# Optimization experiments

Measured on AMD Instinct MI355X. Metric: run time of the kernel, lower is better.

Reference implementation:

```python
import jax, jax.numpy as jnp
import numpy as np

EMBED_DIM = 128
N_CLASSES = 5
NX = 1024
NY = 1024


def setup_inputs() -> dict:
    key = jax.random.key(0)
    k1, k2 = jax.random.split(key)
    z_x = jax.random.normal(k1, (NX, EMBED_DIM), dtype=jnp.float32)
    z_y = jax.random.normal(k2, (NY, EMBED_DIM), dtype=jnp.float32)
    # Parameter init exactly as in __init__ for the L1 compare
    ex = 2 * np.sqrt(2 / np.pi) * EMBED_DIM
    var = 4 * (1 - 2 / np.pi) * EMBED_DIM
    beta_init = ex / np.sqrt(var)
    theta = jnp.ones((1, N_CLASSES - 1), dtype=jnp.float32) / np.sqrt(var)  # clamped >=0, already positive
    beta = jnp.full((N_CLASSES - 1,), beta_init, dtype=jnp.float32)
    return {"z_x": z_x, "z_y": z_y, "theta": theta, "beta": beta}


def reference(z_x, z_y, theta, beta):
    # L1 compare: s[i,j] = -sum_d |z_x[i,d] - z_y[j,d]|   -> (Nx, Ny)
    s = -jnp.sum(jnp.abs(z_x[:, None, :] - z_y[None, :, :]), axis=-1)
    # SSA: dual softmax soft alignment
    a = jax.nn.softmax(s, axis=1)  # row softmax
    b = jax.nn.softmax(s, axis=0)  # column softmax
    a = a + b - a * b
    a = a / jnp.sum(a)
    # weighted reduction -> scalar similarity
    c = jnp.sum(a * s)
    logits = c * theta + beta  # (1, n_classes-1) broadcast
    return logits.reshape(-1)
```

## Files before the change

### kernel.cpp

```cpp
#include <hip/hip_runtime.h>
#include <math.h>

#define NXC 1024
#define NYC 1024
#define DC  128
#define NCM1 4
#define NBLK 256

#define WS_STILE 0
#define WS_ROWP  1048576
#define WS_COLP  1081344
#define WS_PART  1114112

typedef _Float16 half2v __attribute__((ext_vector_type(2)));
union H2U { half2v h; unsigned u; };

#if defined(__has_builtin)
#if __has_builtin(__builtin_amdgcn_fdot2)
#define HAVE_FDOT2 1
#endif
#endif

__device__ __forceinline__ float absdiff_dot(uint4 xa, uint4 ya, float acc)
{
    const unsigned* xu = (const unsigned*)&xa;
    const unsigned* yu = (const unsigned*)&ya;
    half2v one; one.x = (_Float16)1.f; one.y = (_Float16)1.f;
    #pragma unroll
    for (int q = 0; q < 4; ++q) {
        H2U x, y, d;
        x.u = xu[q]; y.u = yu[q];
        d.h = x.h - y.h;
        d.u &= 0x7FFF7FFFu;
#ifdef HAVE_FDOT2
        acc = __builtin_amdgcn_fdot2(d.h, one, acc, false);
#else
        acc += (float)d.h.x + (float)d.h.y;
#endif
    }
    return acc;
}

__global__ __launch_bounds__(512, 2) void distance_kernel(
    const float* __restrict__ zx, const float* __restrict__ zy,
    float* __restrict__ ws)
{
    __shared__ __align__(16) _Float16 xs[64 * 128];
    __shared__ __align__(16) _Float16 ys[64 * 128];
    __shared__ float cpm[32][64], cpl[32][64];

    float* stile = ws + WS_STILE;
    float* rowp  = ws + WS_ROWP;
    float* colp  = ws + WS_COLP;

    const int t  = threadIdx.x;
    const int bx = blockIdx.x & 15;
    const int by = blockIdx.x >> 4;
    const int x0 = by * 64;
    const int y0 = bx * 64;

    #pragma unroll
    for (int k = 0; k < 2; ++k) {
        int idx = t + k * 512;
        int r   = idx >> 4;
        int j   = idx & 15;
        int off = r * 128 + 8 * (j ^ ((r >> 2) & 7));

        const float4* gx = (const float4*)(zx + (size_t)(x0 + r) * DC + 8 * j);
        float4 xv0 = gx[0], xv1 = gx[1];
        const float4* gy = (const float4*)(zy + (size_t)(y0 + r) * DC + 8 * j);
        float4 yv0 = gy[0], yv1 = gy[1];

        uint4 hx, hy;
        {
            H2U a, b, c, d;
            a.h.x = (_Float16)xv0.x; a.h.y = (_Float16)xv0.y;
            b.h.x = (_Float16)xv0.z; b.h.y = (_Float16)xv0.w;
            c.h.x = (_Float16)xv1.x; c.h.y = (_Float16)xv1.y;
            d.h.x = (_Float16)xv1.z; d.h.y = (_Float16)xv1.w;
            hx.x = a.u; hx.y = b.u; hx.z = c.u; hx.w = d.u;
            a.h.x = (_Float16)yv0.x; a.h.y = (_Float16)yv0.y;
            b.h.x = (_Float16)yv0.z; b.h.y = (_Float16)yv0.w;
            c.h.x = (_Float16)yv1.x; c.h.y = (_Float16)yv1.y;
            d.h.x = (_Float16)yv1.z; d.h.y = (_Float16)yv1.w;
            hy.x = a.u; hy.y = b.u; hy.z = c.u; hy.w = d.u;
        }
        *(uint4*)(xs + off) = hx;
        *(uint4*)(ys + off) = hy;
    }
    __syncthreads();

    const int tx = t & 15;
    const int ty = t >> 4;
    const int xswz = (ty >> 1) & 7;
    const int yswz = tx & 7;

    const _Float16* xb = xs + (2 * ty) * 128;
    const _Float16* yb = ys + (4 * tx) * 128;

    float acc[2][4];
    #pragma unroll
    for (int i = 0; i < 2; ++i)
        #pragma unroll
        for (int j = 0; j < 4; ++j) acc[i][j] = 0.f;

    uint4 xc0 = *(const uint4*)(xb +       8 * (0 ^ xswz));
    uint4 xc1 = *(const uint4*)(xb + 128 + 8 * (0 ^ xswz));
    uint4 yc0 = *(const uint4*)(yb +       8 * (0 ^ yswz));
    uint4 yc1 = *(const uint4*)(yb + 128 + 8 * (0 ^ yswz));
    uint4 yc2 = *(const uint4*)(yb + 256 + 8 * (0 ^ yswz));
    uint4 yc3 = *(const uint4*)(yb + 384 + 8 * (0 ^ yswz));

    #pragma unroll 4
    for (int j = 0; j < 16; ++j) {
        uint4 xa0 = xc0, xa1 = xc1, ya0 = yc0, ya1 = yc1, ya2 = yc2, ya3 = yc3;
        if (j < 15) {
            const int jn = j + 1;
            xc0 = *(const uint4*)(xb +       8 * (jn ^ xswz));
            xc1 = *(const uint4*)(xb + 128 + 8 * (jn ^ xswz));
            yc0 = *(const uint4*)(yb +       8 * (jn ^ yswz));
            yc1 = *(const uint4*)(yb + 128 + 8 * (jn ^ yswz));
            yc2 = *(const uint4*)(yb + 256 + 8 * (jn ^ yswz));
            yc3 = *(const uint4*)(yb + 384 + 8 * (jn ^ yswz));
        }
        acc[0][0] = absdiff_dot(xa0, ya0, acc[0][0]);
        acc[0][1] = absdiff_dot(xa0, ya1, acc[0][1]);
        acc[0][2] = absdiff_dot(xa0, ya2, acc[0][2]);
        acc[0][3] = absdiff_dot(xa0, ya3, acc[0][3]);
        acc[1][0] = absdiff_dot(xa1, ya0, acc[1][0]);
        acc[1][1] = absdiff_dot(xa1, ya1, acc[1][1]);
        acc[1][2] = absdiff_dot(xa1, ya2, acc[1][2]);
        acc[1][3] = absdiff_dot(xa1, ya3, acc[1][3]);
    }

    float sv[2][4];
    #pragma unroll
    for (int i = 0; i < 2; ++i)
        #pragma unroll
        for (int j = 0; j < 4; ++j) sv[i][j] = -acc[i][j];

    {
        float* sb = stile + (size_t)blockIdx.x * 4096 + t * 8;
        *(float4*)(sb)     = make_float4(sv[0][0], sv[0][1], sv[0][2], sv[0][3]);
        *(float4*)(sb + 4) = make_float4(sv[1][0], sv[1][1], sv[1][2], sv[1][3]);
    }

    #pragma unroll
    for (int i = 0; i < 2; ++i) {
        float m = fmaxf(fmaxf(sv[i][0], sv[i][1]), fmaxf(sv[i][2], sv[i][3]));
        float l = __expf(sv[i][0] - m) + __expf(sv[i][1] - m)
                + __expf(sv[i][2] - m) + __expf(sv[i][3] - m);
        #pragma unroll
        for (int off = 1; off < 16; off <<= 1) {
            float mo = __shfl_xor(m, off, 64);
            float lo = __shfl_xor(l, off, 64);
            float nm = fmaxf(m, mo);
            l = l * __expf(m - nm) + lo * __expf(mo - nm);
            m = nm;
        }
        if (tx == 0)
            *(float2*)(rowp + 2 * ((size_t)(x0 + 2 * ty + i) * 16 + bx)) = make_float2(m, l);
    }

    #pragma unroll
    for (int j = 0; j < 4; ++j) {
        float m = fmaxf(sv[0][j], sv[1][j]);
        float l = __expf(sv[0][j] - m) + __expf(sv[1][j] - m);
        cpm[ty][4 * tx + j] = m;
        cpl[ty][4 * tx + j] = l;
    }
    __syncthreads();
    if (t < 64) {
        float m = cpm[0][t], l = cpl[0][t];
        #pragma unroll 8
        for (int k = 1; k < 32; ++k) {
            float mo = cpm[k][t], lo = cpl[k][t];
            float nm = fmaxf(m, mo);
            l = l * __expf(m - nm) + lo * __expf(mo - nm);
            m = nm;
        }
        *(float2*)(colp + 2 * ((size_t)(y0 + t) * 16 + by)) = make_float2(m, l);
    }
}

__global__ __launch_bounds__(512, 2) void reduce_kernel(
    const float* __restrict__ ws_in, float* __restrict__ ws_out)
{
    __shared__ float rm_s[64], rl_s[64], cm_s[64], cl_s[64];
    __shared__ float red0[8], red1[8];

    const float* stile = ws_in + WS_STILE;
    const float* rowp  = ws_in + WS_ROWP;
    const float* colp  = ws_in + WS_COLP;
    float* part = ws_out + WS_PART;

    const int t  = threadIdx.x;
    const int bx = blockIdx.x & 15;
    const int by = blockIdx.x >> 4;
    const int x0 = by * 64;
    const int y0 = bx * 64;

    if (t < 64) {
        const float2* base = (const float2*)(rowp) + (size_t)(x0 + t) * 16;
        float2 p = base[0];
        float m = p.x, l = p.y;
        #pragma unroll
        for (int k = 1; k < 16; ++k) {
            float2 q = base[k];
            float nm = fmaxf(m, q.x);
            l = l * __expf(m - nm) + q.y * __expf(q.x - nm);
            m = nm;
        }
        rm_s[t] = m; rl_s[t] = 1.f / l;
    } else if (t < 128) {
        const float2* base = (const float2*)(colp) + (size_t)(y0 + (t - 64)) * 16;
        float2 p = base[0];
        float m = p.x, l = p.y;
        #pragma unroll
        for (int k = 1; k < 16; ++k) {
            float2 q = base[k];
            float nm = fmaxf(m, q.x);
            l = l * __expf(m - nm) + q.y * __expf(q.x - nm);
            m = nm;
        }
        cm_s[t - 64] = m; cl_s[t - 64] = 1.f / l;
    }
    __syncthreads();

    const int tx = t & 15;
    const int ty = t >> 4;

    const float* sb = stile + (size_t)blockIdx.x * 4096 + t * 8;
    float4 s0 = ((const float4*)sb)[0];
    float4 s1 = ((const float4*)sb)[1];
    float sv[2][4] = {{s0.x, s0.y, s0.z, s0.w}, {s1.x, s1.y, s1.z, s1.w}};

    float S0 = 0.f, S1 = 0.f;
    #pragma unroll
    for (int i = 0; i < 2; ++i) {
        const float rm = rm_s[2 * ty + i];
        const float rl = rl_s[2 * ty + i];
        #pragma unroll
        for (int j = 0; j < 4; ++j) {
            const float cm = cm_s[4 * tx + j];
            const float cl = cl_s[4 * tx + j];
            float s = sv[i][j];
            float a = __expf(s - rm) * rl;
            float b = __expf(s - cm) * cl;
            float w = a + b - a * b;
            S0 += w;
            S1 += w * s;
        }
    }
    #pragma unroll
    for (int off = 32; off; off >>= 1) {
        S0 += __shfl_xor(S0, off, 64);
        S1 += __shfl_xor(S1, off, 64);
    }
    {
        const int wave = t >> 6, lane = t & 63;
        if (lane == 0) { red0[wave] = S0; red1[wave] = S1; }
    }
    __syncthreads();
    if (t == 0) {
        float t0 = 0.f, t1 = 0.f;
        #pragma unroll
        for (int w = 0; w < 8; ++w) { t0 += red0[w]; t1 += red1[w]; }
        *(float2*)(part + 2 * blockIdx.x) = make_float2(t0, t1);
    }
}

__global__ __launch_bounds__(256) void finalize_kernel(
    const float* __restrict__ ws,
    const float* __restrict__ theta, const float* __restrict__ beta,
    float* __restrict__ out)
{
    __shared__ float red0[4], red1[4];
    const float* part = ws + WS_PART;
    const int t = threadIdx.x;

    float2 p = ((const float2*)part)[t];
    float S0 = p.x, S1 = p.y;
    #pragma unroll
    for (int off = 32; off; off >>= 1) {
        S0 += __shfl_xor(S0, off, 64);
        S1 += __shfl_xor(S1, off, 64);
    }
    const int wave = t >> 6, lane = t & 63;
    if (lane == 0) { red0[wave] = S0; red1[wave] = S1; }
    __syncthreads();
    if (t < NCM1) {
        float t0 = red0[0] + red0[1] + red0[2] + red0[3];
        float t1 = red1[0] + red1[1] + red1[2] + red1[3];
        float c = t1 / t0;
        out[t] = c * theta[t] + beta[t];
    }
}

extern "C" void kernel_launch(void* const* d_in, const int* in_sizes, int n_in,
                              void* d_out, int out_size, void* d_ws, size_t ws_size,
                              hipStream_t stream)
{
    const float* zx    = (const float*)d_in[0];
    const float* zy    = (const float*)d_in[1];
    const float* theta = (const float*)d_in[2];
    const float* beta  = (const float*)d_in[3];
    float* out = (float*)d_out;
    float* ws  = (float*)d_ws;

    distance_kernel<<<NBLK, 512, 0, stream>>>(zx, zy, ws);
    reduce_kernel<<<NBLK, 512, 0, stream>>>(ws, ws);
    finalize_kernel<<<1, 256, 0, stream>>>(ws, theta, beta, out);
}
```

Measured before the change: 77.15 us.

## Fuse finalize into reduce via last-block atomic counter and parallelize partial merges

New measurement: 81.51 us. 5.6% more time.

```diff
diff --git a/kernel.cpp b/kernel.cpp
--- a/kernel.cpp
+++ b/kernel.cpp
@@ -11,9 +11,11 @@
 #define WS_ROWP  1048576
 #define WS_COLP  1081344
 #define WS_PART  1114112
+#define WS_CNT   1114624
 
 typedef _Float16 half2v __attribute__((ext_vector_type(2)));
 union H2U { half2v h; unsigned u; };
+union F2U { float2 f; unsigned long long u; };
 
 #if defined(__has_builtin)
 #if __has_builtin(__builtin_amdgcn_fdot2)
@@ -58,6 +60,9 @@
     const int by = blockIdx.x >> 4;
     const int x0 = by * 64;
     const int y0 = bx * 64;
+
+    if (blockIdx.x == 0 && t == 0)
+        ((int*)ws)[WS_CNT] = 0;
 
     #pragma unroll
     for (int k = 0; k < 2; ++k) {
@@ -114,15 +119,14 @@
     #pragma unroll 4
     for (int j = 0; j < 16; ++j) {
         uint4 xa0 = xc0, xa1 = xc1, ya0 = yc0, ya1 = yc1, ya2 = yc2, ya3 = yc3;
-        if (j < 15) {
-            const int jn = j + 1;
-            xc0 = *(const uint4*)(xb +       8 * (jn ^ xswz));
-            xc1 = *(const uint4*)(xb + 128 + 8 * (jn ^ xswz));
-            yc0 = *(const uint4*)(yb +       8 * (jn ^ yswz));
-            yc1 = *(const uint4*)(yb + 128 + 8 * (jn ^ yswz));
-            yc2 = *(const uint4*)(yb + 256 + 8 * (jn ^ yswz));
-            yc3 = *(const uint4*)(yb + 384 + 8 * (jn ^ yswz));
-        }
+        const int jn = (j + 1) & 15;
+        xc0 = *(const uint4*)(xb +       8 * (jn ^ xswz));
+        xc1 = *(const uint4*)(xb + 128 + 8 * (jn ^ xswz));
+        yc0 = *(const uint4*)(yb +       8 * (jn ^ yswz));
+        yc1 = *(const uint4*)(yb + 128 + 8 * (jn ^ yswz));
+        yc2 = *(const uint4*)(yb + 256 + 8 * (jn ^ yswz));
+        yc3 = *(const uint4*)(yb + 384 + 8 * (jn ^ yswz));
+
         acc[0][0] = absdiff_dot(xa0, ya0, acc[0][0]);
         acc[0][1] = absdiff_dot(xa0, ya1, acc[0][1]);
         acc[0][2] = absdiff_dot(xa0, ya2, acc[0][2]);
@@ -184,15 +188,19 @@
 }
 
 __global__ __launch_bounds__(512, 2) void reduce_kernel(
-    const float* __restrict__ ws_in, float* __restrict__ ws_out)
+    float* __restrict__ ws,
+    const float* __restrict__ theta, const float* __restrict__ beta,
+    float* __restrict__ out)
 {
     __shared__ float rm_s[64], rl_s[64], cm_s[64], cl_s[64];
     __shared__ float red0[8], red1[8];
-
-    const float* stile = ws_in + WS_STILE;
-    const float* rowp  = ws_in + WS_ROWP;
-    const float* colp  = ws_in + WS_COLP;
-    float* part = ws_out + WS_PART;
+    __shared__ int last_s;
+
+    const float* stile = ws + WS_STILE;
+    const float4* rowp4 = (const float4*)(ws + WS_ROWP);
+    const float4* colp4 = (const float4*)(ws + WS_COLP);
+    float* part = ws + WS_PART;
+    int*   cnt  = (int*)ws + WS_CNT;
 
     const int t  = threadIdx.x;
     const int bx = blockIdx.x & 15;
@@ -200,39 +208,44 @@
     const int x0 = by * 64;
     const int y0 = bx * 64;
 
-    if (t < 64) {
-        const float2* base = (const float2*)(rowp) + (size_t)(x0 + t) * 16;
-        float2 p = base[0];
-        float m = p.x, l = p.y;
-        #pragma unroll
-        for (int k = 1; k < 16; ++k) {
-            float2 q = base[k];
-            float nm = fmaxf(m, q.x);
-            l = l * __expf(m - nm) + q.y * __expf(q.x - nm);
-            m = nm;
-        }
-        rm_s[t] = m; rl_s[t] = 1.f / l;
-    } else if (t < 128) {
-        const float2* base = (const float2*)(colp) + (size_t)(y0 + (t - 64)) * 16;
-        float2 p = base[0];
-        float m = p.x, l = p.y;
-        #pragma unroll
-        for (int k = 1; k < 16; ++k) {
-            float2 q = base[k];
-            float nm = fmaxf(m, q.x);
-            l = l * __expf(m - nm) + q.y * __expf(q.x - nm);
-            m = nm;
-        }
-        cm_s[t - 64] = m; cl_s[t - 64] = 1.f / l;
-    }
-    __syncthreads();
-
-    const int tx = t & 15;
-    const int ty = t >> 4;
-
     const float* sb = stile + (size_t)blockIdx.x * 4096 + t * 8;
     float4 s0 = ((const float4*)sb)[0];
     float4 s1 = ((const float4*)sb)[1];
+
+    const int item  = t >> 3;
+    const int chunk = t & 7;
+    {
+        float4 q = rowp4[(size_t)(x0 + item) * 8 + chunk];
+        float m = fmaxf(q.x, q.z);
+        float l = q.y * __expf(q.x - m) + q.w * __expf(q.z - m);
+        #pragma unroll
+        for (int off = 1; off < 8; off <<= 1) {
+            float mo = __shfl_xor(m, off, 64);
+            float lo = __shfl_xor(l, off, 64);
+            float nm = fmaxf(m, mo);
+            l = l * __expf(m - nm) + lo * __expf(mo - nm);
+            m = nm;
+        }
+        if (chunk == 0) { rm_s[item] = m; rl_s[item] = 1.f / l; }
+    }
+    {
+        float4 q = colp4[(size_t)(y0 + item) * 8 + chunk];
+        float m = fmaxf(q.x, q.z);
+        float l = q.y * __expf(q.x - m) + q.w * __expf(q.z - m);
+        #pragma unroll
+        for (int off = 1; off < 8; off <<= 1) {
+            float mo = __shfl_xor(m, off, 64);
+            float lo = __shfl_xor(l, off, 64);
+            float nm = fmaxf(m, mo);
+            l = l * __expf(m - nm) + lo * __expf(mo - nm);
+            m = nm;
+        }
+        if (chunk == 0) { cm_s[item] = m; cl_s[item] = 1.f / l; }
+    }
+    __syncthreads();
+
+    const int tx = t & 15;
+    const int ty = t >> 4;
     float sv[2][4] = {{s0.x, s0.y, s0.z, s0.w}, {s1.x, s1.y, s1.z, s1.w}};
 
     float S0 = 0.f, S1 = 0.f;
@@ -267,33 +280,36 @@
         #pragma unroll
         for (int w = 0; w < 8; ++w) { t0 += red0[w]; t1 += red1[w]; }
         *(float2*)(part + 2 * blockIdx.x) = make_float2(t0, t1);
-    }
-}
-
-__global__ __launch_bounds__(256) void finalize_kernel(
-    const float* __restrict__ ws,
-    const float* __restrict__ theta, const float* __restrict__ beta,
-    float* __restrict__ out)
-{
-    __shared__ float red0[4], red1[4];
-    const float* part = ws + WS_PART;
-    const int t = threadIdx.x;
-
-    float2 p = ((const float2*)part)[t];
-    float S0 = p.x, S1 = p.y;
-    #pragma unroll
-    for (int off = 32; off; off >>= 1) {
-        S0 += __shfl_xor(S0, off, 64);
-        S1 += __shfl_xor(S1, off, 64);
-    }
-    const int wave = t >> 6, lane = t & 63;
-    if (lane == 0) { red0[wave] = S0; red1[wave] = S1; }
-    __syncthreads();
-    if (t < NCM1) {
-        float t0 = red0[0] + red0[1] + red0[2] + red0[3];
-        float t1 = red1[0] + red1[1] + red1[2] + red1[3];
-        float c = t1 / t0;
-        out[t] = c * theta[t] + beta[t];
+        __threadfence();
+        int old = __hip_atomic_fetch_add(cnt, 1, __ATOMIC_ACQ_REL, __HIP_MEMORY_SCOPE_AGENT);
+        last_s = (old == NBLK - 1);
+    }
+    __syncthreads();
+
+    if (last_s) {
+        float S0f = 0.f, S1f = 0.f;
+        if (t < NBLK) {
+            F2U u;
+            u.u = __hip_atomic_load((const unsigned long long*)(part + 2 * t),
+                                    __ATOMIC_RELAXED, __HIP_MEMORY_SCOPE_AGENT);
+            S0f = u.f.x; S1f = u.f.y;
+        }
+        #pragma unroll
+        for (int off = 32; off; off >>= 1) {
+            S0f += __shfl_xor(S0f, off, 64);
+            S1f += __shfl_xor(S1f, off, 64);
+        }
+        {
+            const int wave = t >> 6, lane = t & 63;
+            if (lane == 0) { red0[wave] = S0f; red1[wave] = S1f; }
+        }
+        __syncthreads();
+        if (t < NCM1) {
+            float t0 = red0[0] + red0[1] + red0[2] + red0[3];
+            float t1 = red1[0] + red1[1] + red1[2] + red1[3];
+            float c = t1 / t0;
+            out[t] = c * theta[t] + beta[t];
+        }
     }
 }
 
@@ -309,6 +325,5 @@
     float* ws  = (float*)d_ws;
 
     distance_kernel<<<NBLK, 512, 0, stream>>>(zx, zy, ws);
-    reduce_kernel<<<NBLK, 512, 0, stream>>>(ws, ws);
-    finalize_kernel<<<1, 256, 0, stream>>>(ws, theta, beta, out);
+    reduce_kernel<<<NBLK, 512, 0, stream>>>(ws, theta, beta, out);
 }
```

## Split distance tiles into half-width blocks and parallelize reduce-stage partial merges

Applied to the files above, without the earlier changes.

Result: no change. 76.67 us (-0.6%).

```diff
diff --git a/kernel.cpp b/kernel.cpp
--- a/kernel.cpp
+++ b/kernel.cpp
@@ -5,12 +5,13 @@
 #define NYC 1024
 #define DC  128
 #define NCM1 4
-#define NBLK 256
+#define NTILE 256
+#define NBLKA 512
 
 #define WS_STILE 0
 #define WS_ROWP  1048576
-#define WS_COLP  1081344
-#define WS_PART  1114112
+#define WS_COLP  1114112
+#define WS_PART  1146880
 
 typedef _Float16 half2v __attribute__((ext_vector_type(2)));
 union H2U { half2v h; unsigned u; };
@@ -41,59 +42,70 @@
     return acc;
 }
 
-__global__ __launch_bounds__(512, 2) void distance_kernel(
+__global__ __launch_bounds__(256, 2) void distance_kernel(
     const float* __restrict__ zx, const float* __restrict__ zy,
     float* __restrict__ ws)
 {
     __shared__ __align__(16) _Float16 xs[64 * 128];
-    __shared__ __align__(16) _Float16 ys[64 * 128];
-    __shared__ float cpm[32][64], cpl[32][64];
+    __shared__ __align__(16) _Float16 ys[32 * 128];
+    __shared__ float cpm[32][32], cpl[32][32];
 
     float* stile = ws + WS_STILE;
     float* rowp  = ws + WS_ROWP;
     float* colp  = ws + WS_COLP;
 
-    const int t  = threadIdx.x;
-    const int bx = blockIdx.x & 15;
-    const int by = blockIdx.x >> 4;
-    const int x0 = by * 64;
-    const int y0 = bx * 64;
-
-    #pragma unroll
-    for (int k = 0; k < 2; ++k) {
-        int idx = t + k * 512;
+    const int t    = threadIdx.x;
+    const int tile = blockIdx.x >> 1;
+    const int h    = blockIdx.x & 1;
+    const int bx   = tile & 15;
+    const int by   = tile >> 4;
+    const int x0   = by * 64;
+    const int y0   = bx * 64 + h * 32;
+
+    #pragma unroll
+    for (int k = 0; k < 4; ++k) {
+        int idx = t + k * 256;
         int r   = idx >> 4;
         int j   = idx & 15;
         int off = r * 128 + 8 * (j ^ ((r >> 2) & 7));
-
         const float4* gx = (const float4*)(zx + (size_t)(x0 + r) * DC + 8 * j);
-        float4 xv0 = gx[0], xv1 = gx[1];
-        const float4* gy = (const float4*)(zy + (size_t)(y0 + r) * DC + 8 * j);
-        float4 yv0 = gy[0], yv1 = gy[1];
-
-        uint4 hx, hy;
+        float4 v0 = gx[0], v1 = gx[1];
+        uint4 hx;
         {
             H2U a, b, c, d;
-            a.h.x = (_Float16)xv0.x; a.h.y = (_Float16)xv0.y;
-            b.h.x = (_Float16)xv0.z; b.h.y = (_Float16)xv0.w;
-            c.h.x = (_Float16)xv1.x; c.h.y = (_Float16)xv1.y;
-            d.h.x = (_Float16)xv1.z; d.h.y = (_Float16)xv1.w;
+            a.h.x = (_Float16)v0.x; a.h.y = (_Float16)v0.y;
+            b.h.x = (_Float16)v0.z; b.h.y = (_Float16)v0.w;
+            c.h.x = (_Float16)v1.x; c.h.y = (_Float16)v1.y;
+            d.h.x = (_Float16)v1.z; d.h.y = (_Float16)v1.w;
             hx.x = a.u; hx.y = b.u; hx.z = c.u; hx.w = d.u;
-            a.h.x = (_Float16)yv0.x; a.h.y = (_Float16)yv0.y;
-            b.h.x = (_Float16)yv0.z; b.h.y = (_Float16)yv0.w;
-            c.h.x = (_Float16)yv1.x; c.h.y = (_Float16)yv1.y;
-            d.h.x = (_Float16)yv1.z; d.h.y = (_Float16)yv1.w;
+        }
+        *(uint4*)(xs + off) = hx;
+    }
+    #pragma unroll
+    for (int k = 0; k < 2; ++k) {
+        int idx = t + k * 256;
+        int r   = idx >> 4;
+        int j   = idx & 15;
+        int off = r * 128 + 8 * (j ^ ((r >> 2) & 7));
+        const float4* gy = (const float4*)(zy + (size_t)(y0 + r) * DC + 8 * j);
+        float4 v0 = gy[0], v1 = gy[1];
+        uint4 hy;
+        {
+            H2U a, b, c, d;
+            a.h.x = (_Float16)v0.x; a.h.y = (_Float16)v0.y;
+            b.h.x = (_Float16)v0.z; b.h.y = (_Float16)v0.w;
+            c.h.x = (_Float16)v1.x; c.h.y = (_Float16)v1.y;
+            d.h.x = (_Float16)v1.z; d.h.y = (_Float16)v1.w;
             hy.x = a.u; hy.y = b.u; hy.z = c.u; hy.w = d.u;
         }
-        *(uint4*)(xs + off) = hx;
         *(uint4*)(ys + off) = hy;
     }
     __syncthreads();
 
-    const int tx = t & 15;
-    const int ty = t >> 4;
+    const int tx = t & 7;
+    const int ty = t >> 3;
     const int xswz = (ty >> 1) & 7;
-    const int yswz = tx & 7;
+    const int yswz = tx;
 
     const _Float16* xb = xs + (2 * ty) * 128;
     const _Float16* yb = ys + (4 * tx) * 128;
@@ -114,15 +126,14 @@
     #pragma unroll 4
     for (int j = 0; j < 16; ++j) {
         uint4 xa0 = xc0, xa1 = xc1, ya0 = yc0, ya1 = yc1, ya2 = yc2, ya3 = yc3;
-        if (j < 15) {
-            const int jn = j + 1;
-            xc0 = *(const uint4*)(xb +       8 * (jn ^ xswz));
-            xc1 = *(const uint4*)(xb + 128 + 8 * (jn ^ xswz));
-            yc0 = *(const uint4*)(yb +       8 * (jn ^ yswz));
-            yc1 = *(const uint4*)(yb + 128 + 8 * (jn ^ yswz));
-            yc2 = *(const uint4*)(yb + 256 + 8 * (jn ^ yswz));
-            yc3 = *(const uint4*)(yb + 384 + 8 * (jn ^ yswz));
-        }
+        const int jn = (j + 1) & 15;
+        xc0 = *(const uint4*)(xb +       8 * (jn ^ xswz));
+        xc1 = *(const uint4*)(xb + 128 + 8 * (jn ^ xswz));
+        yc0 = *(const uint4*)(yb +       8 * (jn ^ yswz));
+        yc1 = *(const uint4*)(yb + 128 + 8 * (jn ^ yswz));
+        yc2 = *(const uint4*)(yb + 256 + 8 * (jn ^ yswz));
+        yc3 = *(const uint4*)(yb + 384 + 8 * (jn ^ yswz));
+
         acc[0][0] = absdiff_dot(xa0, ya0, acc[0][0]);
         acc[0][1] = absdiff_dot(xa0, ya1, acc[0][1]);
         acc[0][2] = absdiff_dot(xa0, ya2, acc[0][2]);
@@ -140,7 +151,7 @@
         for (int j = 0; j < 4; ++j) sv[i][j] = -acc[i][j];
 
     {
-        float* sb = stile + (size_t)blockIdx.x * 4096 + t * 8;
+        float* sb = stile + (size_t)tile * 4096 + h * 2048 + t * 8;
         *(float4*)(sb)     = make_float4(sv[0][0], sv[0][1], sv[0][2], sv[0][3]);
         *(float4*)(sb + 4) = make_float4(sv[1][0], sv[1][1], sv[1][2], sv[1][3]);
     }
@@ -151,7 +162,7 @@
         float l = __expf(sv[i][0] - m) + __expf(sv[i][1] - m)
                 + __expf(sv[i][2] - m) + __expf(sv[i][3] - m);
         #pragma unroll
-        for (int off = 1; off < 16; off <<= 1) {
+        for (int off = 1; off < 8; off <<= 1) {
             float mo = __shfl_xor(m, off, 64);
             float lo = __shfl_xor(l, off, 64);
             float nm = fmaxf(m, mo);
@@ -159,7 +170,7 @@
             m = nm;
         }
         if (tx == 0)
-            *(float2*)(rowp + 2 * ((size_t)(x0 + 2 * ty + i) * 16 + bx)) = make_float2(m, l);
+            *(float2*)(rowp + 2 * ((size_t)(x0 + 2 * ty + i) * 32 + bx * 2 + h)) = make_float2(m, l);
     }
 
     #pragma unroll
@@ -170,7 +181,7 @@
         cpl[ty][4 * tx + j] = l;
     }
     __syncthreads();
-    if (t < 64) {
+    if (t < 32) {
         float m = cpm[0][t], l = cpl[0][t];
         #pragma unroll 8
         for (int k = 1; k < 32; ++k) {
@@ -190,60 +201,76 @@
     __shared__ float red0[8], red1[8];
 
     const float* stile = ws_in + WS_STILE;
-    const float* rowp  = ws_in + WS_ROWP;
-    const float* colp  = ws_in + WS_COLP;
+    const float4* rowp4 = (const float4*)(ws_in + WS_ROWP);
+    const float4* colp4 = (const float4*)(ws_in + WS_COLP);
     float* part = ws_out + WS_PART;
 
-    const int t  = threadIdx.x;
-    const int bx = blockIdx.x & 15;
-    const int by = blockIdx.x >> 4;
-    const int x0 = by * 64;
-    const int y0 = bx * 64;
-
-    if (t < 64) {
-        const float2* base = (const float2*)(rowp) + (size_t)(x0 + t) * 16;
-        float2 p = base[0];
-        float m = p.x, l = p.y;
-        #pragma unroll
-        for (int k = 1; k < 16; ++k) {
-            float2 q = base[k];
-            float nm = fmaxf(m, q.x);
-            l = l * __expf(m - nm) + q.y * __expf(q.x - nm);
-            m = nm;
-        }
-        rm_s[t] = m; rl_s[t] = 1.f / l;
-    } else if (t < 128) {
-        const float2* base = (const float2*)(colp) + (size_t)(y0 + (t - 64)) * 16;
-        float2 p = base[0];
-        float m = p.x, l = p.y;
-        #pragma unroll
-        for (int k = 1; k < 16; ++k) {
-            float2 q = base[k];
-            float nm = fmaxf(m, q.x);
-            l = l * __expf(m - nm) + q.y * __expf(q.x - nm);
-            m = nm;
-        }
-        cm_s[t - 64] = m; cl_s[t - 64] = 1.f / l;
-    }
-    __syncthreads();
-
-    const int tx = t & 15;
-    const int ty = t >> 4;
-
-    const float* sb = stile + (size_t)blockIdx.x * 4096 + t * 8;
+    const int t    = threadIdx.x;
+    const int tile = blockIdx.x;
+    const int bx   = tile & 15;
+    const int by   = tile >> 4;
+    const int x0   = by * 64;
+    const int y0   = bx * 64;
+
+    const float* sb = stile + (size_t)tile * 4096 + t * 8;
     float4 s0 = ((const float4*)sb)[0];
     float4 s1 = ((const float4*)sb)[1];
+
+    const int item  = t >> 3;
+    const int lane8 = t & 7;
+
+    {
+        float4 q0 = rowp4[(size_t)(x0 + item) * 16 + 2 * lane8];
+        float4 q1 = rowp4[(size_t)(x0 + item) * 16 + 2 * lane8 + 1];
+        float m = fmaxf(q0.x, q0.z);
+        float l = q0.y * __expf(q0.x - m) + q0.w * __expf(q0.z - m);
+        float m2 = fmaxf(q1.x, q1.z);
+        float l2 = q1.y * __expf(q1.x - m2) + q1.w * __expf(q1.z - m2);
+        float nm = fmaxf(m, m2);
+        l = l * __expf(m - nm) + l2 * __expf(m2 - nm);
+        m = nm;
+        #pragma unroll
+        for (int off = 1; off < 8; off <<= 1) {
+            float mo = __shfl_xor(m, off, 64);
+            float lo = __shfl_xor(l, off, 64);
+            nm = fmaxf(m, mo);
+            l = l * __expf(m - nm) + lo * __expf(mo - nm);
+            m = nm;
+        }
+        if (lane8 == 0) { rm_s[item] = m; rl_s[item] = 1.f / l; }
+    }
+    {
+        float4 q = colp4[(size_t)(y0 + item) * 8 + lane8];
+        float m = fmaxf(q.x, q.z);
+        float l = q.y * __expf(q.x - m) + q.w * __expf(q.z - m);
+        #pragma unroll
+        for (int off = 1; off < 8; off <<= 1) {
+            float mo = __shfl_xor(m, off, 64);
+            float lo = __shfl_xor(l, off, 64);
+            float nm = fmaxf(m, mo);
+            l = l * __expf(m - nm) + lo * __expf(mo - nm);
+            m = nm;
+        }
+        if (lane8 == 0) { cm_s[item] = m; cl_s[item] = 1.f / l; }
+    }
+    __syncthreads();
+
+    const int tp = t & 255;
+    const int hh = t >> 8;
+    const int i0 = 2 * (tp >> 3);
+    const int c0 = 32 * hh + 4 * (tp & 7);
+
     float sv[2][4] = {{s0.x, s0.y, s0.z, s0.w}, {s1.x, s1.y, s1.z, s1.w}};
 
     float S0 = 0.f, S1 = 0.f;
     #pragma unroll
     for (int i = 0; i < 2; ++i) {
-        const float rm = rm_s[2 * ty + i];
-        const float rl = rl_s[2 * ty + i];
+        const float rm = rm_s[i0 + i];
+        const float rl = rl_s[i0 + i];
         #pragma unroll
         for (int j = 0; j < 4; ++j) {
-            const float cm = cm_s[4 * tx + j];
-            const float cl = cl_s[4 * tx + j];
+            const float cm = cm_s[c0 + j];
+            const float cl = cl_s[c0 + j];
             float s = sv[i][j];
             float a = __expf(s - rm) * rl;
             float b = __expf(s - cm) * cl;
@@ -266,7 +293,7 @@
         float t0 = 0.f, t1 = 0.f;
         #pragma unroll
         for (int w = 0; w < 8; ++w) { t0 += red0[w]; t1 += red1[w]; }
-        *(float2*)(part + 2 * blockIdx.x) = make_float2(t0, t1);
+        *(float2*)(part + 2 * tile) = make_float2(t0, t1);
     }
 }
 
@@ -308,7 +335,7 @@
     float* out = (float*)d_out;
     float* ws  = (float*)d_ws;
 
-    distance_kernel<<<NBLK, 512, 0, stream>>>(zx, zy, ws);
-    reduce_kernel<<<NBLK, 512, 0, stream>>>(ws, ws);
+    distance_kernel<<<NBLKA, 256, 0, stream>>>(zx, zy, ws);
+    reduce_kernel<<<NTILE, 512, 0, stream>>>(ws, ws);
     finalize_kernel<<<1, 256, 0, stream>>>(ws, theta, beta, out);
 }
```
